# Performance work log

Hardware: AMD Instinct MI355X
Metric: run time of the kernel (lower is better)

The kernel has to match this reference:

```python
import jax, jax.numpy as jnp
import numpy as np

B, H, S, D = 4, 16, 2048, 64


def setup_inputs() -> dict:
    key = jax.random.key(0)
    kq, kk, kv = jax.random.split(key, 3)
    q = jax.random.normal(kq, (B, H, S, D), dtype=jnp.float32)
    k = jax.random.normal(kk, (B, H, S, D), dtype=jnp.float32)
    v = jax.random.normal(kv, (B, H, S, D), dtype=jnp.float32)
    # causal mask: 1 where position is masked (j > i), matching mask * -1e9 additive convention
    mask = jnp.triu(jnp.ones((S, S), dtype=jnp.float32), k=1)[None, None]  # [1,1,S,S]
    return {"q": q, "k": k, "v": v, "mask": mask}


def reference(q, k, v, mask):
    scale = 1.0 / jnp.sqrt(jnp.asarray(q.shape[-1], dtype=q.dtype))
    # [B,H,S,S] scores
    scores = jnp.einsum('bhqd,bhkd->bhqk', q, k) * scale
    scores = scores + mask * (-1e9)
    attn = jax.nn.softmax(scores, axis=-1)
    return jnp.einsum('bhqk,bhkd->bhqd', attn, v)
```

## Files before the change

kernel.cpp:

```cpp
#include <hip/hip_runtime.h>
#include <hip/hip_bf16.h>

namespace {

constexpr int Bc = 4, Hc = 16, Sc = 2048, Dc = 64;

using bf16x2 = __attribute__((ext_vector_type(2))) __bf16;
using bf16x8 = __attribute__((ext_vector_type(8))) __bf16;
using f32x4  = __attribute__((ext_vector_type(4))) float;
using f32x16 = __attribute__((ext_vector_type(16))) float;
using uint2v = __attribute__((ext_vector_type(2))) unsigned int;
using uint4v = __attribute__((ext_vector_type(4))) unsigned int;

__device__ __forceinline__ float exp2_hw(float x) {
#if __has_builtin(__builtin_amdgcn_exp2f)
  return __builtin_amdgcn_exp2f(x);
#else
  return exp2f(x);
#endif
}

__device__ __forceinline__ unsigned pk_bf16(float a, float b) {
  bf16x2 t = { (__bf16)a, (__bf16)b };
  return __builtin_bit_cast(unsigned, t);
}

__device__ __forceinline__ void pl32swap(unsigned& a, unsigned& b) {
  asm volatile("s_nop 1\n\tv_permlane32_swap_b32 %0, %1\n\ts_nop 1"
               : "+v"(a), "+v"(b));
}
__device__ __forceinline__ void xhalf_pair(float x, float& lo, float& hi) {
  unsigned a, b;
  asm volatile("v_mov_b32 %0, %2\n\t"
               "v_mov_b32 %1, %2\n\t"
               "s_nop 1\n\t"
               "v_permlane32_swap_b32 %0, %1\n\t"
               "s_nop 1"
               : "=&v"(a), "=&v"(b)
               : "v"(x));
  lo = __builtin_bit_cast(float, a);
  hi = __builtin_bit_cast(float, b);
}
__device__ __forceinline__ float xhalf_sum(float x) {
  float lo, hi; xhalf_pair(x, lo, hi); return lo + hi;
}

__device__ __forceinline__ int vswz(int d) { return ((d >> 4) ^ d) & 7; }

__global__ __launch_bounds__(256)
__attribute__((amdgpu_waves_per_eu(2, 2)))
void fattn_kernel(const float* __restrict__ Q, const float* __restrict__ K,
                  const float* __restrict__ V, float* __restrict__ O) {
  const int tid  = threadIdx.x;
  const int wid  = tid >> 6;
  const int lane = tid & 63;
  const int l31  = lane & 31;
  const int hi   = lane >> 5;

  const int d    = blockIdx.x;
  const int xcd  = d & 7;
  const int n    = d >> 3;
  const int j    = n >> 5;
  const int ci   = n & 31;
  const int bh_l = ci & 7;
  const int b    = ci >> 3;
  const int P    = j ? b : (7 - b);
  const int bh   = xcd * 8 + bh_l;

  const int qb  = P * 256;
  const int wq  = qb + wid * 64;
  const int nkb = 4 * P + 4;

  const size_t base = (size_t)bh * (Sc * Dc);
  const float* Qb = Q + base;
  const float* Kb = K + base;
  const float* Vb = V + base;
  float*       Ob = O + base;

  __shared__ __align__(16) __bf16 k_lds[3][64][64];
  __shared__ __align__(16) __bf16 vt_lds[3][64][64];

  const int srow = tid >> 2;
  const int scol = (tid & 3) * 16;
  const int ssw  = (srow & 7) << 3;
  const int vk0  = (tid >> 4) * 4;
  const int vd0  = (tid & 15) * 4;

  constexpr float QSC = 0.125f * 1.44269504088896f;

  f32x4 Rk0, Rk1, Rk2, Rk3, Rv0, Rv1, Rv2, Rv3;

  auto issue_loads = [&](int krow) {
    const float* ksrc = Kb + (size_t)(krow + srow) * Dc + scol;
    Rk0 = *(const f32x4*)ksrc;
    Rk1 = *(const f32x4*)(ksrc + 4);
    Rk2 = *(const f32x4*)(ksrc + 8);
    Rk3 = *(const f32x4*)(ksrc + 12);
    const float* vsrc = Vb + (size_t)(krow + vk0) * Dc + vd0;
    Rv0 = *(const f32x4*)vsrc;
    Rv1 = *(const f32x4*)(vsrc + Dc);
    Rv2 = *(const f32x4*)(vsrc + 2 * Dc);
    Rv3 = *(const f32x4*)(vsrc + 3 * Dc);
  };
  auto write_stage = [&](__bf16 (*kd)[64], __bf16 (*vd)[64]) {
    uint4v w0, w1;
    w0[0] = pk_bf16(Rk0[0], Rk0[1]); w0[1] = pk_bf16(Rk0[2], Rk0[3]);
    w0[2] = pk_bf16(Rk1[0], Rk1[1]); w0[3] = pk_bf16(Rk1[2], Rk1[3]);
    w1[0] = pk_bf16(Rk2[0], Rk2[1]); w1[1] = pk_bf16(Rk2[2], Rk2[3]);
    w1[2] = pk_bf16(Rk3[0], Rk3[1]); w1[3] = pk_bf16(Rk3[2], Rk3[3]);
    *(uint4v*)&kd[srow][scol ^ ssw]       = w0;
    *(uint4v*)&kd[srow][(scol + 8) ^ ssw] = w1;
    #pragma unroll
    for (int e = 0; e < 4; ++e) {
      const int dd = vd0 + e;
      uint2v wv2;
      wv2[0] = pk_bf16(Rv0[e], Rv1[e]);
      wv2[1] = pk_bf16(Rv2[e], Rv3[e]);
      *(uint2v*)&vd[dd][vk0 ^ (vswz(dd) << 3)] = wv2;
    }
  };

  bf16x8 qfA[4], qfB[4];
  #pragma unroll
  for (int g = 0; g < 2; ++g) {
    const float* qrow = Qb + (size_t)(wq + g * 32 + l31) * Dc;
    #pragma unroll
    for (int s = 0; s < 4; ++s) {
      const float* src = qrow + s * 16 + hi * 8;
      f32x4 a0 = *(const f32x4*)src;
      f32x4 a1 = *(const f32x4*)(src + 4);
      uint4v wv;
      wv[0] = pk_bf16(a0[0] * QSC, a0[1] * QSC);
      wv[1] = pk_bf16(a0[2] * QSC, a0[3] * QSC);
      wv[2] = pk_bf16(a1[0] * QSC, a1[1] * QSC);
      wv[3] = pk_bf16(a1[2] * QSC, a1[3] * QSC);
      if (g == 0) qfA[s] = __builtin_bit_cast(bf16x8, wv);
      else        qfB[s] = __builtin_bit_cast(bf16x8, wv);
    }
  }

  f32x16 oA0, oA1, oB0, oB1;
  #pragma unroll
  for (int i = 0; i < 16; ++i) { oA0[i] = 0.f; oA1[i] = 0.f; oB0[i] = 0.f; oB1[i] = 0.f; }
  float lA = 0.f, lB = 0.f;

  auto compute_group = [&](int kbase, const __bf16 (*kc)[64], const __bf16 (*vc)[64],
                           const bf16x8 (&qf)[4], f32x16& o0, f32x16& o1,
                           float& l, int qg) {
    f32x16 s0, s1;
    #pragma unroll
    for (int i = 0; i < 16; ++i) { s0[i] = 0.f; s1[i] = 0.f; }
    const int ksw = (l31 & 7) << 3;
    __builtin_amdgcn_s_setprio(1);
    #pragma unroll
    for (int s = 0; s < 4; ++s) {
      bf16x8 kf = *(const bf16x8*)&kc[l31][(s * 16 + hi * 8) ^ ksw];
      s0 = __builtin_amdgcn_mfma_f32_32x32x16_bf16(kf, qf[s], s0, 0, 0, 0);
    }
    #pragma unroll
    for (int s = 0; s < 4; ++s) {
      bf16x8 kf = *(const bf16x8*)&kc[32 + l31][(s * 16 + hi * 8) ^ ksw];
      s1 = __builtin_amdgcn_mfma_f32_32x32x16_bf16(kf, qf[s], s1, 0, 0, 0);
    }
    __builtin_amdgcn_s_setprio(0);

    if (kbase + 63 > qg) {
      const int q   = qg + l31;
      const int dq0 = q - (kbase + 4 * hi);
      const int dq1 = q - (kbase + 32 + 4 * hi);
      #pragma unroll
      for (int i = 0; i < 16; ++i) {
        const int off = (i & 3) + 8 * (i >> 2);
        if (off > dq0) s0[i] = -1e30f;
        if (off > dq1) s1[i] = -1e30f;
      }
    }

    #pragma unroll
    for (int i = 0; i < 16; ++i) {
      s0[i] = exp2_hw(s0[i]);
      s1[i] = exp2_hw(s1[i]);
    }
    float sm[16];
    #pragma unroll
    for (int i = 0; i < 16; ++i) sm[i] = s0[i] + s1[i];
    #pragma unroll
    for (int st = 8; st > 0; st >>= 1)
      #pragma unroll
      for (int i = 0; i < st; ++i) sm[i] += sm[i + st];
    l += xhalf_sum(sm[0]);

    uint4v wv;
    unsigned t0, t1, t2, t3;
    t0 = pk_bf16(s0[0], s0[1]);  t1 = pk_bf16(s0[2], s0[3]);
    t2 = pk_bf16(s0[4], s0[5]);  t3 = pk_bf16(s0[6], s0[7]);
    pl32swap(t0, t2); pl32swap(t1, t3);
    wv[0] = t0; wv[1] = t1; wv[2] = t2; wv[3] = t3;
    const bf16x8 pf0 = __builtin_bit_cast(bf16x8, wv);
    t0 = pk_bf16(s0[8], s0[9]);   t1 = pk_bf16(s0[10], s0[11]);
    t2 = pk_bf16(s0[12], s0[13]); t3 = pk_bf16(s0[14], s0[15]);
    pl32swap(t0, t2); pl32swap(t1, t3);
    wv[0] = t0; wv[1] = t1; wv[2] = t2; wv[3] = t3;
    const bf16x8 pf1 = __builtin_bit_cast(bf16x8, wv);
    t0 = pk_bf16(s1[0], s1[1]);  t1 = pk_bf16(s1[2], s1[3]);
    t2 = pk_bf16(s1[4], s1[5]);  t3 = pk_bf16(s1[6], s1[7]);
    pl32swap(t0, t2); pl32swap(t1, t3);
    wv[0] = t0; wv[1] = t1; wv[2] = t2; wv[3] = t3;
    const bf16x8 pf2 = __builtin_bit_cast(bf16x8, wv);
    t0 = pk_bf16(s1[8], s1[9]);   t1 = pk_bf16(s1[10], s1[11]);
    t2 = pk_bf16(s1[12], s1[13]); t3 = pk_bf16(s1[14], s1[15]);
    pl32swap(t0, t2); pl32swap(t1, t3);
    wv[0] = t0; wv[1] = t1; wv[2] = t2; wv[3] = t3;
    const bf16x8 pf3 = __builtin_bit_cast(bf16x8, wv);

    const int vc0 = l31, vc1 = 32 + l31;
    const int vs0 = vswz(vc0) << 3, vs1 = vswz(vc1) << 3;
    bf16x8 vf;
    __builtin_amdgcn_s_setprio(1);
    vf = *(const bf16x8*)&vc[vc0][(hi * 8) ^ vs0];
    o0 = __builtin_amdgcn_mfma_f32_32x32x16_bf16(vf, pf0, o0, 0, 0, 0);
    vf = *(const bf16x8*)&vc[vc0][(16 + hi * 8) ^ vs0];
    o0 = __builtin_amdgcn_mfma_f32_32x32x16_bf16(vf, pf1, o0, 0, 0, 0);
    vf = *(const bf16x8*)&vc[vc0][(32 + hi * 8) ^ vs0];
    o0 = __builtin_amdgcn_mfma_f32_32x32x16_bf16(vf, pf2, o0, 0, 0, 0);
    vf = *(const bf16x8*)&vc[vc0][(48 + hi * 8) ^ vs0];
    o0 = __builtin_amdgcn_mfma_f32_32x32x16_bf16(vf, pf3, o0, 0, 0, 0);
    vf = *(const bf16x8*)&vc[vc1][(hi * 8) ^ vs1];
    o1 = __builtin_amdgcn_mfma_f32_32x32x16_bf16(vf, pf0, o1, 0, 0, 0);
    vf = *(const bf16x8*)&vc[vc1][(16 + hi * 8) ^ vs1];
    o1 = __builtin_amdgcn_mfma_f32_32x32x16_bf16(vf, pf1, o1, 0, 0, 0);
    vf = *(const bf16x8*)&vc[vc1][(32 + hi * 8) ^ vs1];
    o1 = __builtin_amdgcn_mfma_f32_32x32x16_bf16(vf, pf2, o1, 0, 0, 0);
    vf = *(const bf16x8*)&vc[vc1][(48 + hi * 8) ^ vs1];
    o1 = __builtin_amdgcn_mfma_f32_32x32x16_bf16(vf, pf3, o1, 0, 0, 0);
    __builtin_amdgcn_s_setprio(0);
  };

  issue_loads(0);
  write_stage(k_lds[0], vt_lds[0]);
  issue_loads(64);
  __syncthreads();

  for (int t = 0; t < nkb; ++t) {
    const int bq = t % 3;
    const int bw = (t + 1) % 3;
    const int kbase = t * 64;

    if (t + 1 < nkb) write_stage(k_lds[bw], vt_lds[bw]);

    if (t + 2 < nkb) issue_loads((t + 2) * 64);

    asm volatile("s_waitcnt lgkmcnt(0)" ::: "memory");
    __builtin_amdgcn_s_barrier();

    if (kbase <= wq + 63) {
      const __bf16 (*kc)[64] = k_lds[bq];
      const __bf16 (*vc)[64] = vt_lds[bq];
      compute_group(kbase, kc, vc, qfA, oA0, oA1, lA, wq);
      compute_group(kbase, kc, vc, qfB, oB0, oB1, lB, wq + 32);
    }
  }

  {
    const float inv = 1.0f / lA;
    float* orow = Ob + (size_t)(wq + l31) * Dc;
    #pragma unroll
    for (int b2 = 0; b2 < 4; ++b2) {
      f32x4 u0, u1;
      #pragma unroll
      for (int e = 0; e < 4; ++e) { u0[e] = oA0[4 * b2 + e] * inv; u1[e] = oA1[4 * b2 + e] * inv; }
      *(f32x4*)(orow + 8 * b2 + 4 * hi)      = u0;
      *(f32x4*)(orow + 32 + 8 * b2 + 4 * hi) = u1;
    }
  }
  {
    const float inv = 1.0f / lB;
    float* orow = Ob + (size_t)(wq + 32 + l31) * Dc;
    #pragma unroll
    for (int b2 = 0; b2 < 4; ++b2) {
      f32x4 u0, u1;
      #pragma unroll
      for (int e = 0; e < 4; ++e) { u0[e] = oB0[4 * b2 + e] * inv; u1[e] = oB1[4 * b2 + e] * inv; }
      *(f32x4*)(orow + 8 * b2 + 4 * hi)      = u0;
      *(f32x4*)(orow + 32 + 8 * b2 + 4 * hi) = u1;
    }
  }
}

}

extern "C" void kernel_launch(void* const* d_in, const int* in_sizes, int n_in,
                              void* d_out, int out_size, void* d_ws, size_t ws_size,
                              hipStream_t stream) {
  const float* q = (const float*)d_in[0];
  const float* k = (const float*)d_in[1];
  const float* v = (const float*)d_in[2];
  float* o = (float*)d_out;
  fattn_kernel<<<dim3(512), dim3(256), 0, stream>>>(q, k, v, o);
}
```

Before: 69.53 us.

## Pair mirrored causal query chunks per wave to balance work and share K fragments

Each wave now owns two 32-row query chunks, cA and 63-cA, so every block carries a balanced share of the causal triangle. This replaces the previous assignment of contiguous 256-row tiles with paired block scheduling. While both chunks are active, the K and V fragments loaded from LDS are reused across two interleaved MFMA chains, which raises ILP and cuts LDS reads. The cost is doubled score registers during the paired phase, a branchy loop body, and a different XCD/block mapping plus a changed launch-bounds form.

```diff
diff --git a/kernel.cpp b/kernel.cpp
--- a/kernel.cpp
+++ b/kernel.cpp
@@ -47,8 +47,7 @@
 
 __device__ __forceinline__ int vswz(int d) { return ((d >> 4) ^ d) & 7; }
 
-__global__ __launch_bounds__(256)
-__attribute__((amdgpu_waves_per_eu(2, 2)))
+__global__ __launch_bounds__(256, 2)
 void fattn_kernel(const float* __restrict__ Q, const float* __restrict__ K,
                   const float* __restrict__ V, float* __restrict__ O) {
   const int tid  = threadIdx.x;
@@ -57,19 +56,18 @@
   const int l31  = lane & 31;
   const int hi   = lane >> 5;
 
-  const int d    = blockIdx.x;
-  const int xcd  = d & 7;
-  const int n    = d >> 3;
-  const int j    = n >> 5;
-  const int ci   = n & 31;
-  const int bh_l = ci & 7;
-  const int b    = ci >> 3;
-  const int P    = j ? b : (7 - b);
-  const int bh   = xcd * 8 + bh_l;
-
-  const int qb  = P * 256;
-  const int wq  = qb + wid * 64;
-  const int nkb = 4 * P + 4;
+  const int flat = blockIdx.x + 8 * blockIdx.y;
+  const int w    = (flat & 7) * 64 + (flat >> 3);
+  const int bp   = w & 7;
+  const int bh   = w >> 3;
+
+  const int cA   = 4 * bp + wid;
+  const int cB   = 63 - cA;
+  const int qA   = 32 * cA;
+  const int qB   = 32 * cB;
+  const int nkbA = (cA >> 1) + 1;
+  const int nkbB = (cB >> 1) + 1;
+  const int Lb   = ((63 - 4 * bp) >> 1) + 1;
 
   const size_t base = (size_t)bh * (Sc * Dc);
   const float* Qb = Q + base;
@@ -112,18 +110,18 @@
     *(uint4v*)&kd[srow][(scol + 8) ^ ssw] = w1;
     #pragma unroll
     for (int e = 0; e < 4; ++e) {
-      const int dd = vd0 + e;
+      const int d = vd0 + e;
       uint2v wv2;
       wv2[0] = pk_bf16(Rv0[e], Rv1[e]);
       wv2[1] = pk_bf16(Rv2[e], Rv3[e]);
-      *(uint2v*)&vd[dd][vk0 ^ (vswz(dd) << 3)] = wv2;
+      *(uint2v*)&vd[d][vk0 ^ (vswz(d) << 3)] = wv2;
     }
   };
 
   bf16x8 qfA[4], qfB[4];
   #pragma unroll
   for (int g = 0; g < 2; ++g) {
-    const float* qrow = Qb + (size_t)(wq + g * 32 + l31) * Dc;
+    const float* qrow = Qb + (size_t)((g ? qB : qA) + l31) * Dc;
     #pragma unroll
     for (int s = 0; s < 4; ++s) {
       const float* src = qrow + s * 16 + hi * 8;
@@ -144,96 +142,42 @@
   for (int i = 0; i < 16; ++i) { oA0[i] = 0.f; oA1[i] = 0.f; oB0[i] = 0.f; oB1[i] = 0.f; }
   float lA = 0.f, lB = 0.f;
 
-  auto compute_group = [&](int kbase, const __bf16 (*kc)[64], const __bf16 (*vc)[64],
-                           const bf16x8 (&qf)[4], f32x16& o0, f32x16& o1,
-                           float& l, int qg) {
-    f32x16 s0, s1;
-    #pragma unroll
-    for (int i = 0; i < 16; ++i) { s0[i] = 0.f; s1[i] = 0.f; }
-    const int ksw = (l31 & 7) << 3;
-    __builtin_amdgcn_s_setprio(1);
-    #pragma unroll
-    for (int s = 0; s < 4; ++s) {
-      bf16x8 kf = *(const bf16x8*)&kc[l31][(s * 16 + hi * 8) ^ ksw];
-      s0 = __builtin_amdgcn_mfma_f32_32x32x16_bf16(kf, qf[s], s0, 0, 0, 0);
-    }
-    #pragma unroll
-    for (int s = 0; s < 4; ++s) {
-      bf16x8 kf = *(const bf16x8*)&kc[32 + l31][(s * 16 + hi * 8) ^ ksw];
-      s1 = __builtin_amdgcn_mfma_f32_32x32x16_bf16(kf, qf[s], s1, 0, 0, 0);
-    }
-    __builtin_amdgcn_s_setprio(0);
-
-    if (kbase + 63 > qg) {
-      const int q   = qg + l31;
-      const int dq0 = q - (kbase + 4 * hi);
-      const int dq1 = q - (kbase + 32 + 4 * hi);
-      #pragma unroll
-      for (int i = 0; i < 16; ++i) {
-        const int off = (i & 3) + 8 * (i >> 2);
-        if (off > dq0) s0[i] = -1e30f;
-        if (off > dq1) s1[i] = -1e30f;
-      }
-    }
-
-    #pragma unroll
-    for (int i = 0; i < 16; ++i) {
-      s0[i] = exp2_hw(s0[i]);
-      s1[i] = exp2_hw(s1[i]);
-    }
-    float sm[16];
-    #pragma unroll
-    for (int i = 0; i < 16; ++i) sm[i] = s0[i] + s1[i];
-    #pragma unroll
-    for (int st = 8; st > 0; st >>= 1)
-      #pragma unroll
-      for (int i = 0; i < st; ++i) sm[i] += sm[i + st];
-    l += xhalf_sum(sm[0]);
-
+  auto build_pf = [&](const f32x16& s0, const f32x16& s1,
+                      bf16x8& pf0, bf16x8& pf1, bf16x8& pf2, bf16x8& pf3) {
     uint4v wv;
     unsigned t0, t1, t2, t3;
     t0 = pk_bf16(s0[0], s0[1]);  t1 = pk_bf16(s0[2], s0[3]);
     t2 = pk_bf16(s0[4], s0[5]);  t3 = pk_bf16(s0[6], s0[7]);
     pl32swap(t0, t2); pl32swap(t1, t3);
     wv[0] = t0; wv[1] = t1; wv[2] = t2; wv[3] = t3;
-    const bf16x8 pf0 = __builtin_bit_cast(bf16x8, wv);
+    pf0 = __builtin_bit_cast(bf16x8, wv);
     t0 = pk_bf16(s0[8], s0[9]);   t1 = pk_bf16(s0[10], s0[11]);
     t2 = pk_bf16(s0[12], s0[13]); t3 = pk_bf16(s0[14], s0[15]);
     pl32swap(t0, t2); pl32swap(t1, t3);
     wv[0] = t0; wv[1] = t1; wv[2] = t2; wv[3] = t3;
-    const bf16x8 pf1 = __builtin_bit_cast(bf16x8, wv);
+    pf1 = __builtin_bit_cast(bf16x8, wv);
     t0 = pk_bf16(s1[0], s1[1]);  t1 = pk_bf16(s1[2], s1[3]);
     t2 = pk_bf16(s1[4], s1[5]);  t3 = pk_bf16(s1[6], s1[7]);
     pl32swap(t0, t2); pl32swap(t1, t3);
     wv[0] = t0; wv[1] = t1; wv[2] = t2; wv[3] = t3;
-    const bf16x8 pf2 = __builtin_bit_cast(bf16x8, wv);
+    pf2 = __builtin_bit_cast(bf16x8, wv);
     t0 = pk_bf16(s1[8], s1[9]);   t1 = pk_bf16(s1[10], s1[11]);
     t2 = pk_bf16(s1[12], s1[13]); t3 = pk_bf16(s1[14], s1[15]);
     pl32swap(t0, t2); pl32swap(t1, t3);
     wv[0] = t0; wv[1] = t1; wv[2] = t2; wv[3] = t3;
-    const bf16x8 pf3 = __builtin_bit_cast(bf16x8, wv);
-
-    const int vc0 = l31, vc1 = 32 + l31;
-    const int vs0 = vswz(vc0) << 3, vs1 = vswz(vc1) << 3;
-    bf16x8 vf;
-    __builtin_amdgcn_s_setprio(1);
-    vf = *(const bf16x8*)&vc[vc0][(hi * 8) ^ vs0];
-    o0 = __builtin_amdgcn_mfma_f32_32x32x16_bf16(vf, pf0, o0, 0, 0, 0);
-    vf = *(const bf16x8*)&vc[vc0][(16 + hi * 8) ^ vs0];
-    o0 = __builtin_amdgcn_mfma_f32_32x32x16_bf16(vf, pf1, o0, 0, 0, 0);
-    vf = *(const bf16x8*)&vc[vc0][(32 + hi * 8) ^ vs0];
-    o0 = __builtin_amdgcn_mfma_f32_32x32x16_bf16(vf, pf2, o0, 0, 0, 0);
-    vf = *(const bf16x8*)&vc[vc0][(48 + hi * 8) ^ vs0];
-    o0 = __builtin_amdgcn_mfma_f32_32x32x16_bf16(vf, pf3, o0, 0, 0, 0);
-    vf = *(const bf16x8*)&vc[vc1][(hi * 8) ^ vs1];
-    o1 = __builtin_amdgcn_mfma_f32_32x32x16_bf16(vf, pf0, o1, 0, 0, 0);
-    vf = *(const bf16x8*)&vc[vc1][(16 + hi * 8) ^ vs1];
-    o1 = __builtin_amdgcn_mfma_f32_32x32x16_bf16(vf, pf1, o1, 0, 0, 0);
-    vf = *(const bf16x8*)&vc[vc1][(32 + hi * 8) ^ vs1];
-    o1 = __builtin_amdgcn_mfma_f32_32x32x16_bf16(vf, pf2, o1, 0, 0, 0);
-    vf = *(const bf16x8*)&vc[vc1][(48 + hi * 8) ^ vs1];
-    o1 = __builtin_amdgcn_mfma_f32_32x32x16_bf16(vf, pf3, o1, 0, 0, 0);
-    __builtin_amdgcn_s_setprio(0);
+    pf3 = __builtin_bit_cast(bf16x8, wv);
+  };
+
+  auto mask_scores = [&](int kbase, int qg, f32x16& s0, f32x16& s1) {
+    const int q   = qg + l31;
+    const int dq0 = q - (kbase + 4 * hi);
+    const int dq1 = q - (kbase + 32 + 4 * hi);
+    #pragma unroll
+    for (int i = 0; i < 16; ++i) {
+      const int off = (i & 3) + 8 * (i >> 2);
+      if (off > dq0) s0[i] = -1e30f;
+      if (off > dq1) s1[i] = -1e30f;
+    }
   };
 
   issue_loads(0);
@@ -241,29 +185,156 @@
   issue_loads(64);
   __syncthreads();
 
-  for (int t = 0; t < nkb; ++t) {
+  for (int t = 0; t < Lb; ++t) {
     const int bq = t % 3;
     const int bw = (t + 1) % 3;
     const int kbase = t * 64;
 
-    if (t + 1 < nkb) write_stage(k_lds[bw], vt_lds[bw]);
-
-    if (t + 2 < nkb) issue_loads((t + 2) * 64);
+    if (t + 1 < Lb) write_stage(k_lds[bw], vt_lds[bw]);
+
+    if (t + 2 < Lb) issue_loads((t + 2) * 64);
 
     asm volatile("s_waitcnt lgkmcnt(0)" ::: "memory");
     __builtin_amdgcn_s_barrier();
 
-    if (kbase <= wq + 63) {
-      const __bf16 (*kc)[64] = k_lds[bq];
-      const __bf16 (*vc)[64] = vt_lds[bq];
-      compute_group(kbase, kc, vc, qfA, oA0, oA1, lA, wq);
-      compute_group(kbase, kc, vc, qfB, oB0, oB1, lB, wq + 32);
+    const __bf16 (*kc)[64] = k_lds[bq];
+    const __bf16 (*vc)[64] = vt_lds[bq];
+    const int ksw = (l31 & 7) << 3;
+    const int vr0 = l31, vr1 = 32 + l31;
+    const int vs0 = vswz(vr0) << 3, vs1 = vswz(vr1) << 3;
+
+    if (t < nkbA) {
+      f32x16 sA0, sA1, sB0, sB1;
+      #pragma unroll
+      for (int i = 0; i < 16; ++i) { sA0[i] = 0.f; sA1[i] = 0.f; sB0[i] = 0.f; sB1[i] = 0.f; }
+      __builtin_amdgcn_s_setprio(1);
+      #pragma unroll
+      for (int s = 0; s < 4; ++s) {
+        bf16x8 kf = *(const bf16x8*)&kc[l31][(s * 16 + hi * 8) ^ ksw];
+        sA0 = __builtin_amdgcn_mfma_f32_32x32x16_bf16(kf, qfA[s], sA0, 0, 0, 0);
+        sB0 = __builtin_amdgcn_mfma_f32_32x32x16_bf16(kf, qfB[s], sB0, 0, 0, 0);
+      }
+      #pragma unroll
+      for (int s = 0; s < 4; ++s) {
+        bf16x8 kf = *(const bf16x8*)&kc[32 + l31][(s * 16 + hi * 8) ^ ksw];
+        sA1 = __builtin_amdgcn_mfma_f32_32x32x16_bf16(kf, qfA[s], sA1, 0, 0, 0);
+        sB1 = __builtin_amdgcn_mfma_f32_32x32x16_bf16(kf, qfB[s], sB1, 0, 0, 0);
+      }
+      __builtin_amdgcn_s_setprio(0);
+
+      if (kbase + 63 > qA) mask_scores(kbase, qA, sA0, sA1);
+
+      #pragma unroll
+      for (int i = 0; i < 16; ++i) {
+        sA0[i] = exp2_hw(sA0[i]); sA1[i] = exp2_hw(sA1[i]);
+        sB0[i] = exp2_hw(sB0[i]); sB1[i] = exp2_hw(sB1[i]);
+      }
+
+      bf16x8 pfA0, pfA1, pfA2, pfA3, pfB0, pfB1, pfB2, pfB3;
+      build_pf(sA0, sA1, pfA0, pfA1, pfA2, pfA3);
+      build_pf(sB0, sB1, pfB0, pfB1, pfB2, pfB3);
+
+      float smA[16], smB[16];
+      #pragma unroll
+      for (int i = 0; i < 16; ++i) { smA[i] = sA0[i] + sA1[i]; smB[i] = sB0[i] + sB1[i]; }
+      #pragma unroll
+      for (int st = 8; st > 0; st >>= 1)
+        #pragma unroll
+        for (int i = 0; i < st; ++i) { smA[i] += smA[i + st]; smB[i] += smB[i + st]; }
+
+      bf16x8 vf;
+      __builtin_amdgcn_s_setprio(1);
+      vf = *(const bf16x8*)&vc[vr0][(hi * 8) ^ vs0];
+      oA0 = __builtin_amdgcn_mfma_f32_32x32x16_bf16(vf, pfA0, oA0, 0, 0, 0);
+      oB0 = __builtin_amdgcn_mfma_f32_32x32x16_bf16(vf, pfB0, oB0, 0, 0, 0);
+      vf = *(const bf16x8*)&vc[vr0][(16 + hi * 8) ^ vs0];
+      oA0 = __builtin_amdgcn_mfma_f32_32x32x16_bf16(vf, pfA1, oA0, 0, 0, 0);
+      oB0 = __builtin_amdgcn_mfma_f32_32x32x16_bf16(vf, pfB1, oB0, 0, 0, 0);
+      vf = *(const bf16x8*)&vc[vr0][(32 + hi * 8) ^ vs0];
+      oA0 = __builtin_amdgcn_mfma_f32_32x32x16_bf16(vf, pfA2, oA0, 0, 0, 0);
+      oB0 = __builtin_amdgcn_mfma_f32_32x32x16_bf16(vf, pfB2, oB0, 0, 0, 0);
+      vf = *(const bf16x8*)&vc[vr0][(48 + hi * 8) ^ vs0];
+      oA0 = __builtin_amdgcn_mfma_f32_32x32x16_bf16(vf, pfA3, oA0, 0, 0, 0);
+      oB0 = __builtin_amdgcn_mfma_f32_32x32x16_bf16(vf, pfB3, oB0, 0, 0, 0);
+      vf = *(const bf16x8*)&vc[vr1][(hi * 8) ^ vs1];
+      oA1 = __builtin_amdgcn_mfma_f32_32x32x16_bf16(vf, pfA0, oA1, 0, 0, 0);
+      oB1 = __builtin_amdgcn_mfma_f32_32x32x16_bf16(vf, pfB0, oB1, 0, 0, 0);
+      vf = *(const bf16x8*)&vc[vr1][(16 + hi * 8) ^ vs1];
+      oA1 = __builtin_amdgcn_mfma_f32_32x32x16_bf16(vf, pfA1, oA1, 0, 0, 0);
+      oB1 = __builtin_amdgcn_mfma_f32_32x32x16_bf16(vf, pfB1, oB1, 0, 0, 0);
+      vf = *(const bf16x8*)&vc[vr1][(32 + hi * 8) ^ vs1];
+      oA1 = __builtin_amdgcn_mfma_f32_32x32x16_bf16(vf, pfA2, oA1, 0, 0, 0);
+      oB1 = __builtin_amdgcn_mfma_f32_32x32x16_bf16(vf, pfB2, oB1, 0, 0, 0);
+      vf = *(const bf16x8*)&vc[vr1][(48 + hi * 8) ^ vs1];
+      oA1 = __builtin_amdgcn_mfma_f32_32x32x16_bf16(vf, pfA3, oA1, 0, 0, 0);
+      oB1 = __builtin_amdgcn_mfma_f32_32x32x16_bf16(vf, pfB3, oB1, 0, 0, 0);
+      __builtin_amdgcn_s_setprio(0);
+
+      lA += xhalf_sum(smA[0]);
+      lB += xhalf_sum(smB[0]);
+    } else if (t < nkbB) {
+      f32x16 s0, s1;
+      #pragma unroll
+      for (int i = 0; i < 16; ++i) { s0[i] = 0.f; s1[i] = 0.f; }
+      __builtin_amdgcn_s_setprio(1);
+      #pragma unroll
+      for (int s = 0; s < 4; ++s) {
+        bf16x8 kf = *(const bf16x8*)&kc[l31][(s * 16 + hi * 8) ^ ksw];
+        s0 = __builtin_amdgcn_mfma_f32_32x32x16_bf16(kf, qfB[s], s0, 0, 0, 0);
+      }
+      #pragma unroll
+      for (int s = 0; s < 4; ++s) {
+        bf16x8 kf = *(const bf16x8*)&kc[32 + l31][(s * 16 + hi * 8) ^ ksw];
+        s1 = __builtin_amdgcn_mfma_f32_32x32x16_bf16(kf, qfB[s], s1, 0, 0, 0);
+      }
+      __builtin_amdgcn_s_setprio(0);
+
+      if (kbase + 63 > qB) mask_scores(kbase, qB, s0, s1);
+
+      #pragma unroll
+      for (int i = 0; i < 16; ++i) {
+        s0[i] = exp2_hw(s0[i]);
+        s1[i] = exp2_hw(s1[i]);
+      }
+
+      bf16x8 pf0, pf1, pf2, pf3;
+      build_pf(s0, s1, pf0, pf1, pf2, pf3);
+
+      float sm[16];
+      #pragma unroll
+      for (int i = 0; i < 16; ++i) sm[i] = s0[i] + s1[i];
+      #pragma unroll
+      for (int st = 8; st > 0; st >>= 1)
+        #pragma unroll
+        for (int i = 0; i < st; ++i) sm[i] += sm[i + st];
+
+      bf16x8 vf;
+      __builtin_amdgcn_s_setprio(1);
+      vf = *(const bf16x8*)&vc[vr0][(hi * 8) ^ vs0];
+      oB0 = __builtin_amdgcn_mfma_f32_32x32x16_bf16(vf, pf0, oB0, 0, 0, 0);
+      vf = *(const bf16x8*)&vc[vr0][(16 + hi * 8) ^ vs0];
+      oB0 = __builtin_amdgcn_mfma_f32_32x32x16_bf16(vf, pf1, oB0, 0, 0, 0);
+      vf = *(const bf16x8*)&vc[vr0][(32 + hi * 8) ^ vs0];
+      oB0 = __builtin_amdgcn_mfma_f32_32x32x16_bf16(vf, pf2, oB0, 0, 0, 0);
+      vf = *(const bf16x8*)&vc[vr0][(48 + hi * 8) ^ vs0];
+      oB0 = __builtin_amdgcn_mfma_f32_32x32x16_bf16(vf, pf3, oB0, 0, 0, 0);
+      vf = *(const bf16x8*)&vc[vr1][(hi * 8) ^ vs1];
+      oB1 = __builtin_amdgcn_mfma_f32_32x32x16_bf16(vf, pf0, oB1, 0, 0, 0);
+      vf = *(const bf16x8*)&vc[vr1][(16 + hi * 8) ^ vs1];
+      oB1 = __builtin_amdgcn_mfma_f32_32x32x16_bf16(vf, pf1, oB1, 0, 0, 0);
+      vf = *(const bf16x8*)&vc[vr1][(32 + hi * 8) ^ vs1];
+      oB1 = __builtin_amdgcn_mfma_f32_32x32x16_bf16(vf, pf2, oB1, 0, 0, 0);
+      vf = *(const bf16x8*)&vc[vr1][(48 + hi * 8) ^ vs1];
+      oB1 = __builtin_amdgcn_mfma_f32_32x32x16_bf16(vf, pf3, oB1, 0, 0, 0);
+      __builtin_amdgcn_s_setprio(0);
+
+      lB += xhalf_sum(sm[0]);
     }
   }
 
   {
     const float inv = 1.0f / lA;
-    float* orow = Ob + (size_t)(wq + l31) * Dc;
+    float* orow = Ob + (size_t)(qA + l31) * Dc;
     #pragma unroll
     for (int b2 = 0; b2 < 4; ++b2) {
       f32x4 u0, u1;
@@ -275,7 +346,7 @@
   }
   {
     const float inv = 1.0f / lB;
-    float* orow = Ob + (size_t)(wq + 32 + l31) * Dc;
+    float* orow = Ob + (size_t)(qB + l31) * Dc;
     #pragma unroll
     for (int b2 = 0; b2 < 4; ++b2) {
       f32x4 u0, u1;
@@ -296,5 +367,6 @@
   const float* k = (const float*)d_in[1];
   const float* v = (const float*)d_in[2];
   float* o = (float*)d_out;
-  fattn_kernel<<<dim3(512), dim3(256), 0, stream>>>(q, k, v, o);
-}
+  dim3 grid(8, Bc * Hc);
+  fattn_kernel<<<grid, dim3(256), 0, stream>>>(q, k, v, o);
+}
```

After: 111.2 us. 1.6x slower.
